# Kernel tuning notes

Hardware: AMD Instinct MI355X
Metric: run time of the kernel (lower is better)

Reference implementation:

```python
import jax, jax.numpy as jnp
import numpy as np

CH = 512
RED = CH // 8  # 64


def setup_inputs() -> dict:
    key = jax.random.key(0)
    ks = jax.random.split(key, 8)
    s = 0.05
    x = jax.random.normal(ks[0], (4, CH, 64, 64), dtype=jnp.float32)
    Wq = jax.random.normal(ks[1], (RED, CH), dtype=jnp.float32) * s
    bq = jnp.zeros((RED,), dtype=jnp.float32)
    Wk = jax.random.normal(ks[2], (RED, CH), dtype=jnp.float32) * s
    bk = jnp.zeros((RED,), dtype=jnp.float32)
    Wv = jax.random.normal(ks[3], (CH, CH), dtype=jnp.float32) * s
    bv = jnp.zeros((CH,), dtype=jnp.float32)
    gamma = jnp.zeros((1,), dtype=jnp.float32)
    return {"x": x, "Wq": Wq, "bq": bq, "Wk": Wk, "bk": bk, "Wv": Wv, "bv": bv, "gamma": gamma}


def reference(x, Wq, bq, Wk, bk, Wv, bv, gamma):
    b, c, h, w = x.shape
    n = h * w
    xf = x.reshape(b, c, n)  # [b, c, n]
    # 1x1 convs == per-pixel linear over channels
    q = jnp.einsum('rc,bcn->bnr', Wq, xf) + bq[None, None, :]   # [b, n, red]
    k = jnp.einsum('rc,bcn->brn', Wk, xf) + bk[None, :, None]   # [b, red, n]
    v = jnp.einsum('oc,bcn->bon', Wv, xf) + bv[None, :, None]   # [b, c, n]
    energy = jnp.einsum('bnr,brm->bnm', q, k)                   # [b, n, n]
    attention = jax.nn.softmax(energy, axis=-1)
    # out[b,c,i] = sum_j v[b,c,j] * attention[b,i,j]
    out = jnp.einsum('bcj,bij->bci', v, attention).reshape(b, c, h, w)
    return gamma[0] * out + x
```

## Files before the change

kernel.cpp:

```cpp
#include <hip/hip_runtime.h>
#include <math.h>

#define CH 512
#define RED 64

typedef __attribute__((ext_vector_type(4))) float f32x4;
typedef long i64;

typedef const __attribute__((address_space(1))) void* gas_t;
typedef __attribute__((address_space(3))) void* las_t;

static __device__ __forceinline__ void gl16(const void* g, void* l) {
    __builtin_amdgcn_global_load_lds((gas_t)g, (las_t)l, 16, 0, 0);
}

static __device__ __forceinline__ unsigned pk4(float a, float b, float c, float d) {
    int w = __builtin_amdgcn_cvt_pk_fp8_f32(a, b, 0, false);
    w = __builtin_amdgcn_cvt_pk_fp8_f32(c, d, w, true);
    return (unsigned)w;
}
static __device__ __forceinline__ unsigned char pk1(float a) {
    return (unsigned char)(__builtin_amdgcn_cvt_pk_fp8_f32(a, a, 0, false) & 0xFF);
}

static __device__ __forceinline__ float fexp2(float v) {
#if __has_builtin(__builtin_amdgcn_exp2f)
    return __builtin_amdgcn_exp2f(v);
#else
    float r; asm("v_exp_f32 %0, %1" : "=v"(r) : "v"(v)); return r;
#endif
}

static __device__ __forceinline__ void barrier_raw() {
    asm volatile("" ::: "memory");
    __builtin_amdgcn_s_barrier();
    asm volatile("" ::: "memory");
}

__global__ __launch_bounds__(128) void prep_w(
    const float* __restrict__ Wq, const float* __restrict__ Wk,
    const float* __restrict__ Wv, unsigned char* __restrict__ Wcat)
{
    const int r = blockIdx.x, t = threadIdx.x;
    const float* src = (r < 64) ? (Wq + (size_t)r * CH)
                     : (r < 128) ? (Wk + (size_t)(r - 64) * CH)
                                 : (Wv + (size_t)(r - 128) * CH);
    const float4 v = *(const float4*)&src[t * 4];
    *(unsigned*)&Wcat[(size_t)r * CH + t * 4] = pk4(v.x, v.y, v.z, v.w);
}

__global__ __launch_bounds__(256) void cast_xt(
    const float* __restrict__ x, unsigned char* __restrict__ xT, int n)
{
    __shared__ float sX[64][65];
    const int b = blockIdx.z, i0 = blockIdx.x * 64, c0 = blockIdx.y * 64;
    const int t = threadIdx.x;
    #pragma unroll
    for (int s = 0; s < 4; ++s) {
        const int id = s * 256 + t, c = id >> 4, seg = id & 15;
        *(float4*)&sX[c][seg * 4] = *(const float4*)&x[((size_t)b * CH + c0 + c) * n + i0 + seg * 4];
    }
    __syncthreads();
    const int i = t >> 2, cp = t & 3;
    uint4 w;
    w.x = pk4(sX[cp*16+ 0][i], sX[cp*16+ 1][i], sX[cp*16+ 2][i], sX[cp*16+ 3][i]);
    w.y = pk4(sX[cp*16+ 4][i], sX[cp*16+ 5][i], sX[cp*16+ 6][i], sX[cp*16+ 7][i]);
    w.z = pk4(sX[cp*16+ 8][i], sX[cp*16+ 9][i], sX[cp*16+10][i], sX[cp*16+11][i]);
    w.w = pk4(sX[cp*16+12][i], sX[cp*16+13][i], sX[cp*16+14][i], sX[cp*16+15][i]);
    *(uint4*)&xT[((size_t)b * n + i0 + i) * CH + c0 + cp * 16] = w;
}

__global__ __launch_bounds__(256, 4) void qkv_gemm(
    const unsigned char* __restrict__ xT, const unsigned char* __restrict__ Wcat,
    const float* __restrict__ bq, const float* __restrict__ bk,
    const float* __restrict__ bv,
    unsigned char* __restrict__ qF, unsigned char* __restrict__ kF,
    unsigned char* __restrict__ v2, int n)
{
    __shared__ char smem[40960];
    const int b = blockIdx.z, i0 = blockIdx.x * 128, o0 = blockIdx.y * 128;
    const int t = threadIdx.x, lane = t & 63;
    const int quad = lane >> 4, l16 = lane & 15;
    const int wrow = (t >> 6) & 1, wcol = t >> 7;

    f32x4 acc[4][4];
    const f32x4 zz = {0.f, 0.f, 0.f, 0.f};
    #pragma unroll
    for (int mi = 0; mi < 4; ++mi)
        #pragma unroll
        for (int ci = 0; ci < 4; ++ci) acc[mi][ci] = zz;

    const unsigned char* Ab = xT + ((size_t)b * n + i0) * CH;
    const unsigned char* Bb = Wcat + (size_t)o0 * CH;

    auto stageChunk = [&](int c0, char* dst) {
        #pragma unroll
        for (int s = 0; s < 5; ++s) {
            const int c = s * 256 + t;
            const bool isA = c < 640;
            const int tc = isA ? c : c - 640;
            const int r = tc / 5, p = (tc % 5) & 3;
            gl16((isA ? Ab : Bb) + (size_t)r * CH + c0 + p * 16,
                 dst + (isA ? 0 : 10240) + (size_t)tc * 16);
        }
    };

    stageChunk(0, smem);
    __syncthreads();
    stageChunk(64, smem + 20480);

    #pragma unroll
    for (int ci = 0; ci < 8; ++ci) {
        char* cb = smem + (ci & 1) * 20480;
        #pragma unroll
        for (int kk = 0; kk < 64; kk += 32) {
            i64 af[4], bf[4];
            #pragma unroll
            for (int mi = 0; mi < 4; ++mi)
                af[mi] = *(const i64*)(cb + (wrow * 64 + mi * 16 + l16) * 80 + kk + quad * 8);
            #pragma unroll
            for (int cj = 0; cj < 4; ++cj)
                bf[cj] = *(const i64*)(cb + 10240 + (wcol * 64 + cj * 16 + l16) * 80 + kk + quad * 8);
            __builtin_amdgcn_s_setprio(1);
            #pragma unroll
            for (int mi = 0; mi < 4; ++mi)
                #pragma unroll
                for (int cj = 0; cj < 4; ++cj)
                    acc[mi][cj] = __builtin_amdgcn_mfma_f32_16x16x32_fp8_fp8(af[mi], bf[cj], acc[mi][cj], 0, 0, 0);
            __builtin_amdgcn_s_setprio(0);
        }
        asm volatile("s_waitcnt lgkmcnt(0)" ::: "memory");
        barrier_raw();
        if (ci + 2 < 8) {
            stageChunk((ci + 2) * 64, cb);
            asm volatile("s_waitcnt vmcnt(5)" ::: "memory");
            __builtin_amdgcn_sched_barrier(0);
            barrier_raw();
        } else if (ci + 1 < 8) {
            asm volatile("s_waitcnt vmcnt(0)" ::: "memory");
            __builtin_amdgcn_sched_barrier(0);
            barrier_raw();
        }
    }

    float bb[4], scl[4];
    #pragma unroll
    for (int ci = 0; ci < 4; ++ci) {
        const int o = wcol * 64 + ci * 16 + l16;
        if (o0 == 0) {
            bb[ci]  = (o < 64) ? bq[o] : bk[o - 64];
            scl[ci] = (o < 64) ? 1.44269504088896f : 1.0f;
        } else {
            bb[ci]  = bv[o0 - 128 + o];
            scl[ci] = 1.0f;
        }
    }
    __syncthreads();
    unsigned char* sE = (unsigned char*)smem;
    if (o0 == 0) {
        #pragma unroll
        for (int mi = 0; mi < 4; ++mi)
            #pragma unroll
            for (int ci = 0; ci < 4; ++ci)
                #pragma unroll
                for (int r = 0; r < 4; ++r)
                    sE[(wrow*64 + mi*16 + quad*4 + r) * 144 + wcol*64 + ci*16 + l16] =
                        pk1((acc[mi][ci][r] + bb[ci]) * scl[ci]);
    } else {
        #pragma unroll
        for (int mi = 0; mi < 4; ++mi)
            #pragma unroll
            for (int ci = 0; ci < 4; ++ci)
                #pragma unroll
                for (int r = 0; r < 4; ++r)
                    sE[(wcol*64 + ci*16 + l16) * 144 + wrow*64 + mi*16 + quad*4 + r] =
                        pk1(acc[mi][ci][r] + bb[ci]);
    }
    __syncthreads();
    if (o0 == 0) {
        #pragma unroll
        for (int u = 0; u < 2; ++u) {
            const int id = u * 256 + t, i = id >> 2, p = id & 3;
            *(uint4*)&qF[((size_t)b * n + i0 + i) * RED + p * 16] = *(const uint4*)&sE[i * 144 + p * 16];
        }
        #pragma unroll
        for (int u = 0; u < 2; ++u) {
            const int id = u * 256 + t, i = id >> 2, p = id & 3;
            *(uint4*)&kF[((size_t)b * n + i0 + i) * RED + p * 16] = *(const uint4*)&sE[i * 144 + 64 + p * 16];
        }
    } else {
        #pragma unroll
        for (int u = 0; u < 4; ++u) {
            const int id = u * 256 + t, o = id >> 3, p = id & 7;
            *(uint4*)&v2[((size_t)b * CH + (o0 - 128) + o) * n + i0 + p * 16] =
                *(const uint4*)&sE[o * 144 + p * 16];
        }
    }
}

__global__ __launch_bounds__(256, 4) void rowmax(
    const unsigned char* __restrict__ qF, const unsigned char* __restrict__ kF,
    unsigned* __restrict__ mKey, int n)
{
    __shared__ char smem[20480];
    const int b = blockIdx.z, i0 = blockIdx.y * 128, j0 = blockIdx.x * 128;
    const int t = threadIdx.x, lane = t & 63;
    const int quad = lane >> 4, l16 = lane & 15;
    const int wrow = (t >> 6) & 1, wcol = t >> 7;

    const unsigned char* Qb = qF + ((size_t)b * n + i0) * RED;
    const unsigned char* Kb = kF + ((size_t)b * n + j0) * RED;
    #pragma unroll
    for (int s = 0; s < 5; ++s) {
        const int c = s * 256 + t;
        const bool isQ = c < 640;
        const int tc = isQ ? c : c - 640;
        const int r = tc / 5, p = (tc % 5) & 3;
        gl16((isQ ? Qb : Kb) + (size_t)r * RED + p * 16,
             smem + (isQ ? 0 : 10240) + (size_t)tc * 16);
    }
    __syncthreads();

    f32x4 acc[4][4];
    const f32x4 zz = {0.f, 0.f, 0.f, 0.f};
    #pragma unroll
    for (int mi = 0; mi < 4; ++mi)
        #pragma unroll
        for (int ci = 0; ci < 4; ++ci) acc[mi][ci] = zz;

    #pragma unroll
    for (int kk = 0; kk < 64; kk += 32) {
        i64 af[4], bf[4];
        #pragma unroll
        for (int mi = 0; mi < 4; ++mi)
            af[mi] = *(const i64*)(smem + (wrow * 64 + mi * 16 + l16) * 80 + kk + quad * 8);
        #pragma unroll
        for (int ci = 0; ci < 4; ++ci)
            bf[ci] = *(const i64*)(smem + 10240 + (wcol * 64 + ci * 16 + l16) * 80 + kk + quad * 8);
        #pragma unroll
        for (int mi = 0; mi < 4; ++mi)
            #pragma unroll
            for (int ci = 0; ci < 4; ++ci)
                acc[mi][ci] = __builtin_amdgcn_mfma_f32_16x16x32_fp8_fp8(af[mi], bf[ci], acc[mi][ci], 0, 0, 0);
    }

    #pragma unroll
    for (int mi = 0; mi < 4; ++mi)
        #pragma unroll
        for (int r = 0; r < 4; ++r) {
            float mx = fmaxf(fmaxf(acc[mi][0][r], acc[mi][1][r]),
                             fmaxf(acc[mi][2][r], acc[mi][3][r]));
            #pragma unroll
            for (int off = 1; off < 16; off <<= 1) mx = fmaxf(mx, __shfl_xor(mx, off));
            if (l16 == 0) {
                union { float f; unsigned u; } cv; cv.f = mx;
                const unsigned key = ((int)cv.u >= 0) ? (cv.u + 0x80000000u) : ~cv.u;
                atomicMax(&mKey[(size_t)b * n + i0 + wrow * 64 + mi * 16 + quad * 4 + r], key);
            }
        }
}

#define STGSZ 20480
#define SPOFF 40960
#define SLOFF 45056

__global__ __launch_bounds__(512, 4) void attn(
    const unsigned char* __restrict__ qF,
    const unsigned char* __restrict__ kF,
    const unsigned char* __restrict__ v2,
    const unsigned* __restrict__ mKey,
    const float* __restrict__ x, const float* __restrict__ gamma,
    float* __restrict__ y, int n)
{
    __shared__ char smem[46080];
    const int b = blockIdx.x >> 1, ch0 = (blockIdx.x & 1) * 256;
    const int i0 = blockIdx.y * 64;
    const int t = threadIdx.x, lane = t & 63, w = t >> 6;
    const int quad = lane >> 4, l16 = lane & 15;
    const int qh = w & 1, g = w >> 1;
    const int sw = (l16 >> 1) & 3;
    const int boff = (quad & 1) * 8;
    const int phalf = quad >> 1;

    const unsigned char* Qb = qF + ((size_t)b * n + i0) * RED;
    const unsigned char* Kb = kF + (size_t)b * n * RED;
    const unsigned char* Vb = v2 + ((size_t)b * CH + ch0) * n;

    auto stage = [&](int jn, char* dst) {
        const int r = t >> 2, s4 = t & 3, gs = s4 ^ ((r >> 1) & 3);
        if (t < 256)
            gl16(Kb + (size_t)(jn + r) * RED + gs * 16, dst + (size_t)t * 16);
        #pragma unroll
        for (int ps = 0; ps < 2; ++ps) {
            const int id = ps * 512 + t, vr = id >> 2, vs = id & 3;
            const int vgs = vs ^ ((vr >> 1) & 3);
            gl16(Vb + (size_t)vr * n + jn + vgs * 16, dst + 4096 + (size_t)id * 16);
        }
    };

    {
        const int r = t >> 2, s4 = t & 3, gs = s4 ^ ((r >> 1) & 3);
        if (t < 256)
            gl16(Qb + (size_t)r * RED + gs * 16, smem + SPOFF + (size_t)t * 16);
        stage(0, smem);
    }
    float mrow[2];
    #pragma unroll
    for (int qt = 0; qt < 2; ++qt) {
        const unsigned u = mKey[(size_t)b * n + i0 + qh * 32 + qt * 16 + l16];
        const unsigned bits = (u >= 0x80000000u) ? (u - 0x80000000u) : ~u;
        union { unsigned u; float f; } cv; cv.u = bits;
        mrow[qt] = cv.f;
    }
    __syncthreads();

    i64 qreg[2][2];
    #pragma unroll
    for (int qt = 0; qt < 2; ++qt) {
        const int row = qh * 32 + qt * 16 + l16;
        #pragma unroll
        for (int kki = 0; kki < 2; ++kki) {
            const int p = (kki * 2 + phalf) ^ sw;
            qreg[qt][kki] = *(const i64*)(smem + SPOFF + row * 64 + p * 16 + boff);
        }
    }
    asm volatile("s_waitcnt lgkmcnt(0)" ::: "memory");
    barrier_raw();

    const int nchunks = n >> 6;
    if (nchunks > 1) stage(64, smem + STGSZ);

    f32x4 acc[2][4];
    const f32x4 zz = {0.f, 0.f, 0.f, 0.f};
    #pragma unroll
    for (int qt = 0; qt < 2; ++qt)
        #pragma unroll
        for (int ct = 0; ct < 4; ++ct) acc[qt][ct] = zz;
    float lacc[2] = {0.f, 0.f};

    for (int c = 0; c < nchunks; ++c) {
        char* cur = smem + (c & 1) * STGSZ;

        f32x4 S[2];
        S[0] = zz; S[1] = zz;
        __builtin_amdgcn_s_setprio(1);
        #pragma unroll
        for (int kki = 0; kki < 2; ++kki) {
            const int p = (kki * 2 + phalf) ^ sw;
            const i64 kf = *(const i64*)(cur + (g * 16 + l16) * 64 + p * 16 + boff);
            #pragma unroll
            for (int qt = 0; qt < 2; ++qt)
                S[qt] = __builtin_amdgcn_mfma_f32_16x16x32_fp8_fp8(kf, qreg[qt][kki], S[qt], 0, 0, 0);
        }
        __builtin_amdgcn_s_setprio(0);
        #pragma unroll
        for (int qt = 0; qt < 2; ++qt) {
            const float e0 = fexp2(S[qt][0] - mrow[qt]);
            const float e1 = fexp2(S[qt][1] - mrow[qt]);
            const float e2 = fexp2(S[qt][2] - mrow[qt]);
            const float e3 = fexp2(S[qt][3] - mrow[qt]);
            lacc[qt] += (e0 + e1) + (e2 + e3);
            const int qrow = qh * 32 + qt * 16 + l16;
            const int pp = g ^ sw;
            *(unsigned*)(smem + SPOFF + qrow * 64 + pp * 16 + quad * 4) = pk4(e0, e1, e2, e3);
        }
        asm volatile("s_waitcnt lgkmcnt(0)" ::: "memory");
        barrier_raw();

        __builtin_amdgcn_s_setprio(1);
        #pragma unroll
        for (int kki = 0; kki < 2; ++kki) {
            const int p = (kki * 2 + phalf) ^ sw;
            i64 vf[4], pf[2];
            #pragma unroll
            for (int ct = 0; ct < 4; ++ct) {
                const int row = g * 64 + ct * 16 + l16;
                vf[ct] = *(const i64*)(cur + 4096 + row * 64 + p * 16 + boff);
            }
            #pragma unroll
            for (int qt = 0; qt < 2; ++qt) {
                const int qrow = qh * 32 + qt * 16 + l16;
                pf[qt] = *(const i64*)(smem + SPOFF + qrow * 64 + p * 16 + boff);
            }
            #pragma unroll
            for (int qt = 0; qt < 2; ++qt)
                #pragma unroll
                for (int ct = 0; ct < 4; ++ct)
                    acc[qt][ct] = __builtin_amdgcn_mfma_f32_16x16x32_fp8_fp8(vf[ct], pf[qt], acc[qt][ct], 0, 0, 0);
        }
        __builtin_amdgcn_s_setprio(0);

        asm volatile("s_waitcnt lgkmcnt(0)" ::: "memory");
        barrier_raw();

        if (c + 2 < nchunks) {
            stage((c + 2) << 6, cur);
            if (w < 4) asm volatile("s_waitcnt vmcnt(3)" ::: "memory");
            else       asm volatile("s_waitcnt vmcnt(2)" ::: "memory");
            __builtin_amdgcn_sched_barrier(0);
            barrier_raw();
        } else if (c + 1 < nchunks) {
            asm volatile("s_waitcnt vmcnt(0)" ::: "memory");
            __builtin_amdgcn_sched_barrier(0);
            barrier_raw();
        }
    }

    float* sL = (float*)(smem + SLOFF);
    #pragma unroll
    for (int qt = 0; qt < 2; ++qt) {
        float v = lacc[qt];
        v += __shfl_xor(v, 16);
        v += __shfl_xor(v, 32);
        lacc[qt] = v;
    }
    if (quad == 0) {
        #pragma unroll
        for (int qt = 0; qt < 2; ++qt) sL[w * 32 + qt * 16 + l16] = lacc[qt];
    }
    __syncthreads();
    float il[2];
    #pragma unroll
    for (int qt = 0; qt < 2; ++qt) {
        const int idx = qt * 16 + l16;
        il[qt] = 1.0f / (sL[qh * 32 + idx] + sL[(2 + qh) * 32 + idx] +
                         sL[(4 + qh) * 32 + idx] + sL[(6 + qh) * 32 + idx]);
    }

    const float gm = gamma[0];
    float* sT = (float*)smem;
    #pragma unroll
    for (int cr = 0; cr < 4; ++cr) {
        __syncthreads();
        if (g == cr) {
            #pragma unroll
            for (int ct = 0; ct < 4; ++ct)
                #pragma unroll
                for (int qt = 0; qt < 2; ++qt)
                    #pragma unroll
                    for (int rr = 0; rr < 4; ++rr)
                        sT[(ct * 16 + quad * 4 + rr) * 68 + qh * 32 + qt * 16 + l16] =
                            acc[qt][ct][rr] * il[qt];
        }
        __syncthreads();
        const int row = t >> 3, seg = (t & 7) * 8;
        const size_t gb = ((size_t)b * CH + ch0 + cr * 64 + row) * n + i0 + seg;
        #pragma unroll
        for (int u = 0; u < 2; ++u) {
            const float4 xv = *(const float4*)&x[gb + u * 4];
            const float* op = &sT[row * 68 + seg + u * 4];
            float4 yv;
            yv.x = gm * op[0] + xv.x;
            yv.y = gm * op[1] + xv.y;
            yv.z = gm * op[2] + xv.z;
            yv.w = gm * op[3] + xv.w;
            *(float4*)&y[gb + u * 4] = yv;
        }
    }
}

extern "C" void kernel_launch(void* const* d_in, const int* in_sizes, int n_in,
                              void* d_out, int out_size, void* d_ws, size_t ws_size,
                              hipStream_t stream) {
    const float* x     = (const float*)d_in[0];
    const float* Wq    = (const float*)d_in[1];
    const float* bq    = (const float*)d_in[2];
    const float* Wk    = (const float*)d_in[3];
    const float* bk    = (const float*)d_in[4];
    const float* Wv    = (const float*)d_in[5];
    const float* bv    = (const float*)d_in[6];
    const float* gamma = (const float*)d_in[7];
    float* y = (float*)d_out;

    const int N = 64 * 64;
    const int B = in_sizes[0] / (CH * N);

    char* ws = (char*)d_ws;
    unsigned char* xT   = (unsigned char*)ws;  ws += (size_t)B * N * CH;
    unsigned char* qF   = (unsigned char*)ws;  ws += (size_t)B * N * RED;
    unsigned char* kF   = (unsigned char*)ws;  ws += (size_t)B * N * RED;
    unsigned char* v2   = (unsigned char*)ws;  ws += (size_t)B * CH * N;
    unsigned char* Wcat = (unsigned char*)ws;  ws += (size_t)640 * CH;
    unsigned* mKey      = (unsigned*)ws;

    hipMemsetAsync(mKey, 0, (size_t)B * N * 4, stream);

    prep_w<<<dim3(640), 128, 0, stream>>>(Wq, Wk, Wv, Wcat);
    cast_xt<<<dim3(N / 64, CH / 64, B), 256, 0, stream>>>(x, xT, N);
    qkv_gemm<<<dim3(N / 128, 5, B), 256, 0, stream>>>(xT, Wcat, bq, bk, bv, qF, kF, v2, N);
    rowmax<<<dim3(N / 128, N / 128, B), 256, 0, stream>>>(qF, kF, mKey, N);
    attn<<<dim3(4 * B / 2, N / 64), 512, 0, stream>>>(qF, kF, v2, mKey, x, gamma, y, N);
}
```

Measured before the change: 222.7 us.

## Restructure attention loop: per-wave P tiles, triple-buffered K/V staging

Reassigns work so each wave owns a 16-row query tile and computes its full 64-column score block, which keeps P in a per-wave LDS region and removes one of the two block barriers per chunk. Staging moves to three rotating buffers so the load for chunk c+2 is issued at the top of the iteration. The row-sum reduction becomes a pure shuffle with no LDS pass. In exchange the kernel needs about 72KB of LDS per block, which may cut occupancy below the launch-bounds target. Each wave also now redoes the QK^T MFMAs for its rows, where before that work was shared across waves.

```diff
diff --git a/kernel.cpp b/kernel.cpp
--- a/kernel.cpp
+++ b/kernel.cpp
@@ -260,9 +260,10 @@
         }
 }
 
-#define STGSZ 20480
-#define SPOFF 40960
-#define SLOFF 45056
+#define BUF1  20480
+#define BUF2  40960
+#define PWOFF 61440
+#define QOFF  69632
 
 __global__ __launch_bounds__(512, 4) void attn(
     const unsigned char* __restrict__ qF,
@@ -272,129 +273,122 @@
     const float* __restrict__ x, const float* __restrict__ gamma,
     float* __restrict__ y, int n)
 {
-    __shared__ char smem[46080];
+    __shared__ char smem[73728];
     const int b = blockIdx.x >> 1, ch0 = (blockIdx.x & 1) * 256;
     const int i0 = blockIdx.y * 64;
     const int t = threadIdx.x, lane = t & 63, w = t >> 6;
     const int quad = lane >> 4, l16 = lane & 15;
-    const int qh = w & 1, g = w >> 1;
+    const int qt4 = w & 3, half = w >> 2;
     const int sw = (l16 >> 1) & 3;
     const int boff = (quad & 1) * 8;
     const int phalf = quad >> 1;
+    const int p0 = phalf ^ sw;
+    const int pX = (l16 & 7) << 3;
+
+    const int kfA = l16 * 64 + p0 * 16 + boff;
+    const int vA  = 4096 + (half * 128 + l16) * 64 + p0 * 16 + boff;
+    const int qA  = QOFF + (qt4 * 16 + l16) * 64 + p0 * 16 + boff;
+    const int pwB = PWOFF + w * 1024 + l16 * 64;
+    const int prA0 = pwB + ((quad * 8) ^ pX);
+    const int prA1 = pwB + ((32 + quad * 8) ^ pX);
 
     const unsigned char* Qb = qF + ((size_t)b * n + i0) * RED;
     const unsigned char* Kb = kF + (size_t)b * n * RED;
     const unsigned char* Vb = v2 + ((size_t)b * CH + ch0) * n;
 
-    auto stage = [&](int jn, char* dst) {
-        const int r = t >> 2, s4 = t & 3, gs = s4 ^ ((r >> 1) & 3);
-        if (t < 256)
-            gl16(Kb + (size_t)(jn + r) * RED + gs * 16, dst + (size_t)t * 16);
-        #pragma unroll
-        for (int ps = 0; ps < 2; ++ps) {
-            const int id = ps * 512 + t, vr = id >> 2, vs = id & 3;
-            const int vgs = vs ^ ((vr >> 1) & 3);
-            gl16(Vb + (size_t)vr * n + jn + vgs * 16, dst + 4096 + (size_t)id * 16);
-        }
-    };
-
+    const int r = t >> 2, s4 = t & 3, gs = s4 ^ ((r >> 1) & 3);
+    const int kDst = t * 16, vDst0 = 4096 + t * 16, vDst1 = 12288 + t * 16;
+    const size_t vHalf = (size_t)128 * n;
+    const unsigned char* kSrc0 = Kb + (size_t)r * RED + gs * 16;
+    const unsigned char* vSrc0 = Vb + (size_t)r * n + gs * 16;
+
+    if (t < 256) {
+        gl16(Qb + (size_t)r * RED + gs * 16, smem + QOFF + kDst);
+        gl16(kSrc0, smem + kDst);
+    }
+    gl16(vSrc0, smem + vDst0);
+    gl16(vSrc0 + vHalf, smem + vDst1);
+
+    float mrow;
     {
-        const int r = t >> 2, s4 = t & 3, gs = s4 ^ ((r >> 1) & 3);
-        if (t < 256)
-            gl16(Qb + (size_t)r * RED + gs * 16, smem + SPOFF + (size_t)t * 16);
-        stage(0, smem);
-    }
-    float mrow[2];
-    #pragma unroll
-    for (int qt = 0; qt < 2; ++qt) {
-        const unsigned u = mKey[(size_t)b * n + i0 + qh * 32 + qt * 16 + l16];
+        const unsigned u = mKey[(size_t)b * n + i0 + qt4 * 16 + l16];
         const unsigned bits = (u >= 0x80000000u) ? (u - 0x80000000u) : ~u;
         union { unsigned u; float f; } cv; cv.u = bits;
-        mrow[qt] = cv.f;
-    }
-    __syncthreads();
-
-    i64 qreg[2][2];
-    #pragma unroll
-    for (int qt = 0; qt < 2; ++qt) {
-        const int row = qh * 32 + qt * 16 + l16;
-        #pragma unroll
-        for (int kki = 0; kki < 2; ++kki) {
-            const int p = (kki * 2 + phalf) ^ sw;
-            qreg[qt][kki] = *(const i64*)(smem + SPOFF + row * 64 + p * 16 + boff);
-        }
-    }
-    asm volatile("s_waitcnt lgkmcnt(0)" ::: "memory");
-    barrier_raw();
+        mrow = cv.f;
+    }
+    __syncthreads();
+
+    i64 qreg[2];
+    qreg[0] = *(const i64*)(smem + qA);
+    qreg[1] = *(const i64*)(smem + (qA ^ 32));
 
     const int nchunks = n >> 6;
-    if (nchunks > 1) stage(64, smem + STGSZ);
-
-    f32x4 acc[2][4];
+    if (nchunks > 1) {
+        if (t < 256) gl16(kSrc0 + 4096, smem + BUF1 + kDst);
+        gl16(vSrc0 + 64, smem + BUF1 + vDst0);
+        gl16(vSrc0 + vHalf + 64, smem + BUF1 + vDst1);
+    }
+    const unsigned char* kP  = kSrc0 + 8192;
+    const unsigned char* vP0 = vSrc0 + 128;
+    const unsigned char* vP1 = vSrc0 + vHalf + 128;
+
+    f32x4 acc[8];
     const f32x4 zz = {0.f, 0.f, 0.f, 0.f};
     #pragma unroll
-    for (int qt = 0; qt < 2; ++qt)
-        #pragma unroll
-        for (int ct = 0; ct < 4; ++ct) acc[qt][ct] = zz;
-    float lacc[2] = {0.f, 0.f};
+    for (int cht = 0; cht < 8; ++cht) acc[cht] = zz;
+    float lacc = 0.f;
+
+    int cur = 0, nx1 = BUF1, nx2 = BUF2;
 
     for (int c = 0; c < nchunks; ++c) {
-        char* cur = smem + (c & 1) * STGSZ;
-
-        f32x4 S[2];
-        S[0] = zz; S[1] = zz;
+        if (c + 2 < nchunks) {
+            if (t < 256) gl16(kP, smem + nx2 + kDst);
+            gl16(vP0, smem + nx2 + vDst0);
+            gl16(vP1, smem + nx2 + vDst1);
+            kP += 4096; vP0 += 64; vP1 += 64;
+        }
+
+        f32x4 S[4];
+        S[0] = zz; S[1] = zz; S[2] = zz; S[3] = zz;
         __builtin_amdgcn_s_setprio(1);
         #pragma unroll
-        for (int kki = 0; kki < 2; ++kki) {
-            const int p = (kki * 2 + phalf) ^ sw;
-            const i64 kf = *(const i64*)(cur + (g * 16 + l16) * 64 + p * 16 + boff);
-            #pragma unroll
-            for (int qt = 0; qt < 2; ++qt)
-                S[qt] = __builtin_amdgcn_mfma_f32_16x16x32_fp8_fp8(kf, qreg[qt][kki], S[qt], 0, 0, 0);
+        for (int jt = 0; jt < 4; ++jt) {
+            const i64 kf0 = *(const i64*)(smem + cur + kfA + jt * 1024);
+            const i64 kf1 = *(const i64*)(smem + cur + (kfA ^ 32) + jt * 1024);
+            S[jt] = __builtin_amdgcn_mfma_f32_16x16x32_fp8_fp8(kf0, qreg[0], S[jt], 0, 0, 0);
+            S[jt] = __builtin_amdgcn_mfma_f32_16x16x32_fp8_fp8(kf1, qreg[1], S[jt], 0, 0, 0);
         }
         __builtin_amdgcn_s_setprio(0);
-        #pragma unroll
-        for (int qt = 0; qt < 2; ++qt) {
-            const float e0 = fexp2(S[qt][0] - mrow[qt]);
-            const float e1 = fexp2(S[qt][1] - mrow[qt]);
-            const float e2 = fexp2(S[qt][2] - mrow[qt]);
-            const float e3 = fexp2(S[qt][3] - mrow[qt]);
-            lacc[qt] += (e0 + e1) + (e2 + e3);
-            const int qrow = qh * 32 + qt * 16 + l16;
-            const int pp = g ^ sw;
-            *(unsigned*)(smem + SPOFF + qrow * 64 + pp * 16 + quad * 4) = pk4(e0, e1, e2, e3);
+
+        #pragma unroll
+        for (int jt = 0; jt < 4; ++jt) {
+            const float e0 = fexp2(S[jt][0] - mrow);
+            const float e1 = fexp2(S[jt][1] - mrow);
+            const float e2 = fexp2(S[jt][2] - mrow);
+            const float e3 = fexp2(S[jt][3] - mrow);
+            lacc += (e0 + e1) + (e2 + e3);
+            *(unsigned*)(smem + pwB + ((jt * 16 + quad * 4) ^ pX)) = pk4(e0, e1, e2, e3);
         }
         asm volatile("s_waitcnt lgkmcnt(0)" ::: "memory");
-        barrier_raw();
+        __builtin_amdgcn_sched_barrier(0);
+
+        const i64 pb0 = *(const i64*)(smem + prA0);
+        const i64 pb1 = *(const i64*)(smem + prA1);
 
         __builtin_amdgcn_s_setprio(1);
         #pragma unroll
-        for (int kki = 0; kki < 2; ++kki) {
-            const int p = (kki * 2 + phalf) ^ sw;
-            i64 vf[4], pf[2];
-            #pragma unroll
-            for (int ct = 0; ct < 4; ++ct) {
-                const int row = g * 64 + ct * 16 + l16;
-                vf[ct] = *(const i64*)(cur + 4096 + row * 64 + p * 16 + boff);
-            }
-            #pragma unroll
-            for (int qt = 0; qt < 2; ++qt) {
-                const int qrow = qh * 32 + qt * 16 + l16;
-                pf[qt] = *(const i64*)(smem + SPOFF + qrow * 64 + p * 16 + boff);
-            }
-            #pragma unroll
-            for (int qt = 0; qt < 2; ++qt)
-                #pragma unroll
-                for (int ct = 0; ct < 4; ++ct)
-                    acc[qt][ct] = __builtin_amdgcn_mfma_f32_16x16x32_fp8_fp8(vf[ct], pf[qt], acc[qt][ct], 0, 0, 0);
+        for (int cht = 0; cht < 8; ++cht) {
+            const i64 vf0 = *(const i64*)(smem + cur + vA + cht * 1024);
+            acc[cht] = __builtin_amdgcn_mfma_f32_16x16x32_fp8_fp8(vf0, pb0, acc[cht], 0, 0, 0);
+        }
+        #pragma unroll
+        for (int cht = 0; cht < 8; ++cht) {
+            const i64 vf1 = *(const i64*)(smem + cur + (vA ^ 32) + cht * 1024);
+            acc[cht] = __builtin_amdgcn_mfma_f32_16x16x32_fp8_fp8(vf1, pb1, acc[cht], 0, 0, 0);
         }
         __builtin_amdgcn_s_setprio(0);
 
-        asm volatile("s_waitcnt lgkmcnt(0)" ::: "memory");
-        barrier_raw();
-
         if (c + 2 < nchunks) {
-            stage((c + 2) << 6, cur);
             if (w < 4) asm volatile("s_waitcnt vmcnt(3)" ::: "memory");
             else       asm volatile("s_waitcnt vmcnt(2)" ::: "memory");
             __builtin_amdgcn_sched_barrier(0);
@@ -404,43 +398,25 @@
             __builtin_amdgcn_sched_barrier(0);
             barrier_raw();
         }
-    }
-
-    float* sL = (float*)(smem + SLOFF);
-    #pragma unroll
-    for (int qt = 0; qt < 2; ++qt) {
-        float v = lacc[qt];
-        v += __shfl_xor(v, 16);
-        v += __shfl_xor(v, 32);
-        lacc[qt] = v;
-    }
-    if (quad == 0) {
-        #pragma unroll
-        for (int qt = 0; qt < 2; ++qt) sL[w * 32 + qt * 16 + l16] = lacc[qt];
-    }
-    __syncthreads();
-    float il[2];
-    #pragma unroll
-    for (int qt = 0; qt < 2; ++qt) {
-        const int idx = qt * 16 + l16;
-        il[qt] = 1.0f / (sL[qh * 32 + idx] + sL[(2 + qh) * 32 + idx] +
-                         sL[(4 + qh) * 32 + idx] + sL[(6 + qh) * 32 + idx]);
-    }
+        const int tmp = cur; cur = nx1; nx1 = nx2; nx2 = tmp;
+    }
+
+    lacc += __shfl_xor(lacc, 16);
+    lacc += __shfl_xor(lacc, 32);
+    const float il = 1.0f / lacc;
 
     const float gm = gamma[0];
     float* sT = (float*)smem;
     #pragma unroll
     for (int cr = 0; cr < 4; ++cr) {
         __syncthreads();
-        if (g == cr) {
-            #pragma unroll
-            for (int ct = 0; ct < 4; ++ct)
+        if (half == (cr >> 1)) {
+            #pragma unroll
+            for (int k = 0; k < 4; ++k)
                 #pragma unroll
-                for (int qt = 0; qt < 2; ++qt)
-                    #pragma unroll
-                    for (int rr = 0; rr < 4; ++rr)
-                        sT[(ct * 16 + quad * 4 + rr) * 68 + qh * 32 + qt * 16 + l16] =
-                            acc[qt][ct][rr] * il[qt];
+                for (int rr = 0; rr < 4; ++rr)
+                    sT[(k * 16 + quad * 4 + rr) * 68 + qt4 * 16 + l16] =
+                        acc[(cr & 1) * 4 + k][rr] * il;
         }
         __syncthreads();
         const int row = t >> 3, seg = (t & 7) * 8;
@@ -489,5 +465,5 @@
     cast_xt<<<dim3(N / 64, CH / 64, B), 256, 0, stream>>>(x, xT, N);
     qkv_gemm<<<dim3(N / 128, 5, B), 256, 0, stream>>>(xT, Wcat, bq, bk, bv, qF, kF, v2, N);
     rowmax<<<dim3(N / 128, N / 128, B), 256, 0, stream>>>(qF, kF, mKey, N);
-    attn<<<dim3(4 * B / 2, N / 64), 512, 0, stream>>>(qF, kF, v2, mKey, x, gamma, y, N);
-}
+    attn<<<dim3(2 * B, N / 64), 512, 0, stream>>>(qF, kF, v2, mKey, x, gamma, y, N);
+}
```

New measurement: 256.9 us. +15.3%, slower.
